# Kernel tuning notes

Measured on AMD Instinct MI355X. Metric: run time of the kernel, lower is better.

## Reference

```python
import jax, jax.numpy as jnp
import numpy as np

N_STEPS = 2   # n_steps; n_head = 1 (module is only consistent for a single head)
NEG_SLOPE = 0.2


def setup_inputs() -> dict:
    key = jax.random.key(0)
    ks = jax.random.split(key, 6)
    B, C, N = 8, 2048, 2048  # N must equal input_dim (coefs*out broadcast requirement)
    s = 1.0 / np.sqrt(C).astype(np.float32)
    x = jax.random.normal(ks[0], (B, C, N), jnp.float32)
    Wa = jax.random.normal(ks[1], (C, C), jnp.float32) * s   # conv1x1, no bias
    Wb = jax.random.normal(ks[2], (C,), jnp.float32) * s     # conv1x1 -> 1 channel
    bb = jnp.zeros((1,), jnp.float32)
    Wc = jax.random.normal(ks[3], (C,), jnp.float32) * s
    bc = jnp.zeros((1,), jnp.float32)
    bias = jnp.zeros((C,), jnp.float32)                      # self.bias (zeros)
    return dict(x=x, Wa=Wa, Wb=Wb, bb=bb, Wc=Wc, bc=bc, bias=bias)


def _head_attention(out, Wa, Wb, bb, Wc, bc, bias):
    # dropout p=0.0 -> identity
    h = jnp.einsum('oc,bcn->bon', Wa, out)            # [B,C,N] conv1x1 projection
    t1 = jnp.einsum('c,bcn->bn', Wb, h) + bb          # [B,N]
    t2 = jnp.einsum('c,bcn->bn', Wc, h) + bc          # [B,N]
    z = t1[:, None, :] + t2[:, :, None]               # [B,N,N] additive outer-sum
    z = jnp.where(z >= 0, z, NEG_SLOPE * z)           # leaky_relu(0.2)
    # torch F.softmax with no dim on a 3D tensor uses legacy dim=0 (batch dim)
    coefs = jax.nn.softmax(z, axis=0)
    re = coefs * h + bias                             # bias broadcasts over last axis
    return re                                         # [B,N,N] (== [B,C,N] since N==C)


def reference(x, Wa, Wb, bb, Wc, bc, bias):
    out = x
    for _ in range(N_STEPS):
        # n_head == 1: stack of one head then mean is the head itself
        out = _head_attention(out, Wa, Wb, bb, Wc, bc, bias)
    return out
```

## Files before the change

kernel.cpp:

```cpp
#include <hip/hip_runtime.h>
#include <hip/hip_bf16.h>

typedef unsigned short ushort_t;
typedef __attribute__((ext_vector_type(8))) short bf16x8;
typedef __attribute__((ext_vector_type(4))) float f32x4;
typedef __attribute__((ext_vector_type(8))) unsigned short u16x8;
typedef __attribute__((ext_vector_type(4))) unsigned short u16x4;

#define NDIM 2048
#define BDIM 8

__device__ __forceinline__ float bf2f(unsigned short u) {
  union { unsigned int i; float f; } v; v.i = ((unsigned int)u) << 16; return v.f;
}
__device__ __forceinline__ unsigned short f2bf(float f) {
  union { float f; unsigned int i; } v; v.f = f;
  unsigned int x = v.i;
  x += 0x7fffu + ((x >> 16) & 1u);
  return (unsigned short)(x >> 16);
}

__device__ __forceinline__ void gload16(const void* g, void* l) {
  __builtin_amdgcn_global_load_lds(
      (const __attribute__((address_space(1))) void*)g,
      (__attribute__((address_space(3))) void*)l,
      16, 0, 0);
}

__global__ __launch_bounds__(256) void convert_bf16(const float* __restrict__ src,
                                                    unsigned short* __restrict__ dst, int n) {
  int i = (blockIdx.x * 256 + threadIdx.x) * 4;
  if (i < n) {
    f32x4 v = *(const f32x4*)&src[i];
    u16x4 w;
    #pragma unroll
    for (int k = 0; k < 4; ++k) w[k] = f2bf(v[k]);
    *(u16x4*)&dst[i] = w;
  }
}

__global__ __launch_bounds__(256) void transpose_convert(const float* __restrict__ x,
                                                         unsigned short* __restrict__ dst) {
  __shared__ float tile[64][65];
  const int b  = blockIdx.z;
  const int n0 = blockIdx.x * 64;
  const int c0 = blockIdx.y * 64;
  const int tr = threadIdx.x >> 4;
  const int tc = threadIdx.x & 15;
  const float* src = x + ((size_t)b * NDIM + c0) * NDIM + n0;
  #pragma unroll
  for (int p = 0; p < 4; ++p) {
    int r = p * 16 + tr;
    f32x4 v = *(const f32x4*)&src[(size_t)r * NDIM + tc * 4];
    #pragma unroll
    for (int k = 0; k < 4; ++k) tile[r][tc * 4 + k] = v[k];
  }
  __syncthreads();
  unsigned short* d = dst + ((size_t)b * NDIM + n0) * NDIM + c0;
  #pragma unroll
  for (int p = 0; p < 4; ++p) {
    int r = p * 16 + tr;
    u16x4 w;
    #pragma unroll
    for (int k = 0; k < 4; ++k) w[k] = f2bf(tile[tc * 4 + k][r]);
    *(u16x4*)&d[(size_t)r * NDIM + tc * 4] = w;
  }
}

__global__ __launch_bounds__(256) void weff1(const float* __restrict__ Wa,
                                             const float* __restrict__ Wb,
                                             const float* __restrict__ Wc,
                                             float* __restrict__ part) {
  int c  = blockIdx.x * 256 + threadIdx.x;
  int o0 = blockIdx.y * 128;
  float ab = 0.f, ac = 0.f;
  for (int o = o0; o < o0 + 128; ++o) {
    float w = Wa[(size_t)o * NDIM + c];
    ab = fmaf(Wb[o], w, ab);
    ac = fmaf(Wc[o], w, ac);
  }
  part[(size_t)(blockIdx.y * 2 + 0) * NDIM + c] = ab;
  part[(size_t)(blockIdx.y * 2 + 1) * NDIM + c] = ac;
}
__global__ __launch_bounds__(256) void weff2(const float* __restrict__ part,
                                             float* __restrict__ wbe, float* __restrict__ wce) {
  int c = blockIdx.x * 256 + threadIdx.x;
  float ab = 0.f, ac = 0.f;
  #pragma unroll
  for (int i = 0; i < 16; ++i) {
    ab += part[(size_t)(i * 2 + 0) * NDIM + c];
    ac += part[(size_t)(i * 2 + 1) * NDIM + c];
  }
  wbe[c] = ab; wce[c] = ac;
}

__global__ __launch_bounds__(256) void t_kernel(const unsigned short* __restrict__ curT,
                                                const float* __restrict__ wbe,
                                                const float* __restrict__ wce,
                                                const float* __restrict__ bb,
                                                const float* __restrict__ bc,
                                                float* __restrict__ t1, float* __restrict__ t2) {
  int row  = blockIdx.x * 4 + (threadIdx.x >> 6);
  int lane = threadIdx.x & 63;
  const unsigned short* r = curT + (size_t)row * NDIM;
  float a1 = 0.f, a2 = 0.f;
  #pragma unroll
  for (int p = 0; p < 4; ++p) {
    int c0 = p * 512 + lane * 8;
    u16x8 v = *(const u16x8*)&r[c0];
    f32x4 w1a = *(const f32x4*)&wbe[c0];
    f32x4 w1b = *(const f32x4*)&wbe[c0 + 4];
    f32x4 w2a = *(const f32x4*)&wce[c0];
    f32x4 w2b = *(const f32x4*)&wce[c0 + 4];
    #pragma unroll
    for (int j = 0; j < 4; ++j) {
      float xv = bf2f(v[j]);
      a1 = fmaf(w1a[j], xv, a1);
      a2 = fmaf(w2a[j], xv, a2);
    }
    #pragma unroll
    for (int j = 0; j < 4; ++j) {
      float xv = bf2f(v[4 + j]);
      a1 = fmaf(w1b[j], xv, a1);
      a2 = fmaf(w2b[j], xv, a2);
    }
  }
  #pragma unroll
  for (int off = 32; off > 0; off >>= 1) {
    a1 += __shfl_xor(a1, off);
    a2 += __shfl_xor(a2, off);
  }
  if (lane == 0) { t1[row] = a1 + bb[0]; t2[row] = a2 + bc[0]; }
}

__global__ __launch_bounds__(256) void s_kernel(const float* __restrict__ t1,
                                                const float* __restrict__ t2,
                                                float* __restrict__ S) {
  int n = blockIdx.x * 256 + threadIdx.x;
  int o = blockIdx.y;
  float acc = 0.f;
  #pragma unroll
  for (int b = 0; b < BDIM; ++b) {
    float z = t1[b * NDIM + n] + t2[b * NDIM + o];
    z = z >= 0.f ? z : 0.2f * z;
    acc += __expf(z);
  }
  S[(size_t)o * NDIM + n] = __logf(acc);
}

__global__ __launch_bounds__(512, 2) void gemm_fused(
    const unsigned short* __restrict__ A,
    const unsigned short* __restrict__ Bt,
    const float* __restrict__ t1, const float* __restrict__ t2,
    const float* __restrict__ S,  const float* __restrict__ bias,
    unsigned short* __restrict__ outT,
    float* __restrict__ outF,
    int write_f32) {
  __shared__ __align__(16) unsigned short sbuf[4 * 16384];

  const int tid  = threadIdx.x;
  const int lane = tid & 63;
  const int w    = tid >> 6;
  const int wr   = w >> 2;
  const int wc   = w & 3;
  const int bn0  = blockIdx.x * 256;
  const int bm0  = blockIdx.y * 256;
  const int bz   = blockIdx.z;
  const unsigned short* Bb = Bt + (size_t)bz * NDIM * NDIM;

  f32x4 acc[8][4];
  #pragma unroll
  for (int m = 0; m < 8; ++m)
    #pragma unroll
    for (int n = 0; n < 4; ++n) acc[m][n] = (f32x4){0.f, 0.f, 0.f, 0.f};

  const int sr = lane >> 2;
  const int sc = lane & 3;
  const int r0 = (w * 2 + 0) * 16 + sr;
  const int r1 = (w * 2 + 1) * 16 + sr;
  const int sg = sc ^ ((r0 >> 1) & 3);
  const unsigned short* a0 = A  + (size_t)(bm0 + r0) * NDIM + sg * 8;
  const unsigned short* a1 = A  + (size_t)(bm0 + r1) * NDIM + sg * 8;
  const unsigned short* b0 = Bb + (size_t)(bn0 + r0) * NDIM + sg * 8;
  const unsigned short* b1 = Bb + (size_t)(bn0 + r1) * NDIM + sg * 8;

  auto stageA = [&](int kt, int buf) {
    gload16(a0 + kt, &sbuf[buf * 16384 + (w * 2 + 0) * 512]);
    gload16(a1 + kt, &sbuf[buf * 16384 + (w * 2 + 1) * 512]);
  };
  auto stageB = [&](int kt, int buf) {
    gload16(b0 + kt, &sbuf[buf * 16384 + 8192 + (w * 2 + 0) * 512]);
    gload16(b1 + kt, &sbuf[buf * 16384 + 8192 + (w * 2 + 1) * 512]);
  };

  const int fr = lane & 15;
  const int fs = lane >> 4;
  const int sp = (fs ^ ((fr >> 1) & 3)) * 8;

  stageA(0, 0);  stageB(0, 0);
  stageA(32, 1); stageB(32, 1);
  stageA(64, 2); stageB(64, 2);
  asm volatile("s_waitcnt vmcnt(8)" ::: "memory");
  __builtin_amdgcn_s_barrier();

  for (int t4 = 0; t4 < 64; t4 += 4) {
    #pragma unroll
    for (int u = 0; u < 4; ++u) {
      const int t  = t4 + u;
      const int cb = u;
      const int nb = (u + 3) & 3;
      const int tc = (t + 3 > 63) ? 63 : (t + 3);
      const int ktn = tc * 32;
      const unsigned short* Ab = &sbuf[cb * 16384];
      const unsigned short* Bl = &sbuf[cb * 16384 + 8192];

      bf16x8 av[4], bv[4];
      #pragma unroll
      for (int m = 0; m < 4; ++m)
        av[m] = *(const bf16x8*)&Ab[(wr * 128 + m * 16 + fr) * 32 + sp];
      #pragma unroll
      for (int n = 0; n < 4; ++n)
        bv[n] = *(const bf16x8*)&Bl[(wc * 64 + n * 16 + fr) * 32 + sp];
      stageA(ktn, nb);
      __builtin_amdgcn_s_barrier();
      __builtin_amdgcn_s_setprio(1);
      #pragma unroll
      for (int m = 0; m < 4; ++m)
        #pragma unroll
        for (int n = 0; n < 4; ++n)
          acc[m][n] = __builtin_amdgcn_mfma_f32_16x16x32_bf16(av[m], bv[n], acc[m][n], 0, 0, 0);
      __builtin_amdgcn_s_setprio(0);
      __builtin_amdgcn_s_barrier();

      #pragma unroll
      for (int m = 0; m < 4; ++m)
        av[m] = *(const bf16x8*)&Ab[(wr * 128 + (m + 4) * 16 + fr) * 32 + sp];
      stageB(ktn, nb);
      __builtin_amdgcn_s_barrier();
      __builtin_amdgcn_s_setprio(1);
      #pragma unroll
      for (int m = 0; m < 4; ++m)
        #pragma unroll
        for (int n = 0; n < 4; ++n)
          acc[m + 4][n] = __builtin_amdgcn_mfma_f32_16x16x32_bf16(av[m], bv[n], acc[m + 4][n], 0, 0, 0);
      __builtin_amdgcn_s_setprio(0);
      asm volatile("s_waitcnt vmcnt(8)" ::: "memory");
      __builtin_amdgcn_s_barrier();
    }
  }

  float* sT1f = (float*)&sbuf[3 * 16384];
  float* sT2f = sT1f + 256;
  if (tid < 256) sT1f[tid] = t1[bz * NDIM + bn0 + tid];
  else           sT2f[tid - 256] = t2[bz * NDIM + bm0 + (tid - 256)];
  __syncthreads();

  const int lr4 = fs * 4;
  #pragma unroll
  for (int m = 0; m < 8; ++m) {
    #pragma unroll
    for (int n = 0; n < 4; ++n) {
      const int oo = wr * 128 + m * 16 + lr4;
      const int nn = wc * 64 + n * 16 + fr;
      const int o  = bm0 + oo;
      const int ng = bn0 + nn;
      const float tz1  = sT1f[nn];
      const float bval = bias[ng];
      if (write_f32) {
        #pragma unroll
        for (int r = 0; r < 4; ++r) {
          float z = tz1 + sT2f[oo + r];
          z = z >= 0.f ? z : 0.2f * z;
          float coef = __expf(z - S[(size_t)(o + r) * NDIM + ng]);
          outF[(size_t)bz * NDIM * NDIM + (size_t)(o + r) * NDIM + ng] =
              fmaf(coef, acc[m][n][r], bval);
        }
      } else {
        u16x4 wv;
        #pragma unroll
        for (int r = 0; r < 4; ++r) {
          float z = tz1 + sT2f[oo + r];
          z = z >= 0.f ? z : 0.2f * z;
          float coef = __expf(z - S[(size_t)(o + r) * NDIM + ng]);
          wv[r] = f2bf(fmaf(coef, acc[m][n][r], bval));
        }
        *(u16x4*)&outT[(size_t)bz * NDIM * NDIM + (size_t)ng * NDIM + o] = wv;
      }
    }
  }
}

extern "C" void kernel_launch(void* const* d_in, const int* in_sizes, int n_in,
                              void* d_out, int out_size, void* d_ws, size_t ws_size,
                              hipStream_t stream) {
  const float* x    = (const float*)d_in[0];
  const float* Wa   = (const float*)d_in[1];
  const float* Wb   = (const float*)d_in[2];
  const float* bb   = (const float*)d_in[3];
  const float* Wc   = (const float*)d_in[4];
  const float* bc   = (const float*)d_in[5];
  const float* bias = (const float*)d_in[6];
  float* out = (float*)d_out;

  char* ws = (char*)d_ws;
  unsigned short* curA = (unsigned short*)ws; ws += (size_t)BDIM * NDIM * NDIM * 2;
  unsigned short* curB = (unsigned short*)ws; ws += (size_t)BDIM * NDIM * NDIM * 2;
  unsigned short* WaB  = (unsigned short*)ws; ws += (size_t)NDIM * NDIM * 2;
  float* t1   = (float*)ws; ws += (size_t)BDIM * NDIM * 4;
  float* t2   = (float*)ws; ws += (size_t)BDIM * NDIM * 4;
  float* wbe  = (float*)ws; ws += NDIM * 4;
  float* wce  = (float*)ws; ws += NDIM * 4;
  float* part = (float*)ws; ws += (size_t)32 * NDIM * 4;
  float* S    = (float*)ws; ws += (size_t)NDIM * NDIM * 4;

  convert_bf16<<<4096, 256, 0, stream>>>(Wa, WaB, NDIM * NDIM);
  transpose_convert<<<dim3(32, 32, BDIM), 256, 0, stream>>>(x, curA);
  weff1<<<dim3(8, 16), 256, 0, stream>>>(Wa, Wb, Wc, part);
  weff2<<<8, 256, 0, stream>>>(part, wbe, wce);

  for (int step = 0; step < 2; ++step) {
    const unsigned short* cur = step ? curB : curA;
    t_kernel<<<(BDIM * NDIM) / 4, 256, 0, stream>>>(cur, wbe, wce, bb, bc, t1, t2);
    s_kernel<<<dim3(NDIM / 256, NDIM), 256, 0, stream>>>(t1, t2, S);
    gemm_fused<<<dim3(8, 8, BDIM), 512, 0, stream>>>(
        WaB, cur, t1, t2, S, bias, curB, out, step);
  }
}
```

Baseline: 388.4 us.

## Remap GEMM blocks across XCDs and merge the two MFMA phases per k-step

The 3D grid becomes a 1D grid of 512 blocks. Block ids are remapped so that tiles sharing the same Wa row-block (bm) and batch region land on the same XCD, which should improve L2 reuse. The inner k-loop issues both A and B async stages up front, loads all LDS fragments at once, and runs all 32 MFMAs in a single phase. That removes two of the three barriers per k-step. The costs are more live fragment registers, and the per-u-iteration stage-then-single-barrier pattern needs the 4-buffer ring depth to stay race-free. The epilogue scratch moves to buffer 0.

```diff
diff --git a/kernel.cpp b/kernel.cpp
--- a/kernel.cpp
+++ b/kernel.cpp
@@ -158,14 +158,21 @@
     int write_f32) {
   __shared__ __align__(16) unsigned short sbuf[4 * 16384];
 
+  const int id   = blockIdx.x;
+  const int xcd  = id & 7;
+  const int j    = id >> 3;
+  const int bm   = (xcd >> 1) * 2 + (j & 1);
+  const int idx  = (xcd & 1) * 32 + (j >> 1);
+  const int bz   = idx >> 3;
+  const int bn   = idx & 7;
+  const int bn0  = bn * 256;
+  const int bm0  = bm * 256;
+
   const int tid  = threadIdx.x;
   const int lane = tid & 63;
   const int w    = tid >> 6;
   const int wr   = w >> 2;
   const int wc   = w & 3;
-  const int bn0  = blockIdx.x * 256;
-  const int bm0  = blockIdx.y * 256;
-  const int bz   = blockIdx.z;
   const unsigned short* Bb = Bt + (size_t)bz * NDIM * NDIM;
 
   f32x4 acc[8][4];
@@ -214,42 +221,39 @@
       const unsigned short* Ab = &sbuf[cb * 16384];
       const unsigned short* Bl = &sbuf[cb * 16384 + 8192];
 
-      bf16x8 av[4], bv[4];
+      stageA(ktn, nb);
+      stageB(ktn, nb);
+
+      bf16x8 av0[4], bv[4], av1[4];
       #pragma unroll
       for (int m = 0; m < 4; ++m)
-        av[m] = *(const bf16x8*)&Ab[(wr * 128 + m * 16 + fr) * 32 + sp];
+        av0[m] = *(const bf16x8*)&Ab[(wr * 128 + m * 16 + fr) * 32 + sp];
       #pragma unroll
       for (int n = 0; n < 4; ++n)
         bv[n] = *(const bf16x8*)&Bl[(wc * 64 + n * 16 + fr) * 32 + sp];
-      stageA(ktn, nb);
-      __builtin_amdgcn_s_barrier();
+      #pragma unroll
+      for (int m = 0; m < 4; ++m)
+        av1[m] = *(const bf16x8*)&Ab[(wr * 128 + (m + 4) * 16 + fr) * 32 + sp];
+
       __builtin_amdgcn_s_setprio(1);
       #pragma unroll
       for (int m = 0; m < 4; ++m)
         #pragma unroll
         for (int n = 0; n < 4; ++n)
-          acc[m][n] = __builtin_amdgcn_mfma_f32_16x16x32_bf16(av[m], bv[n], acc[m][n], 0, 0, 0);
-      __builtin_amdgcn_s_setprio(0);
-      __builtin_amdgcn_s_barrier();
-
-      #pragma unroll
-      for (int m = 0; m < 4; ++m)
-        av[m] = *(const bf16x8*)&Ab[(wr * 128 + (m + 4) * 16 + fr) * 32 + sp];
-      stageB(ktn, nb);
-      __builtin_amdgcn_s_barrier();
-      __builtin_amdgcn_s_setprio(1);
+          acc[m][n] = __builtin_amdgcn_mfma_f32_16x16x32_bf16(av0[m], bv[n], acc[m][n], 0, 0, 0);
       #pragma unroll
       for (int m = 0; m < 4; ++m)
         #pragma unroll
         for (int n = 0; n < 4; ++n)
-          acc[m + 4][n] = __builtin_amdgcn_mfma_f32_16x16x32_bf16(av[m], bv[n], acc[m + 4][n], 0, 0, 0);
+          acc[m + 4][n] = __builtin_amdgcn_mfma_f32_16x16x32_bf16(av1[m], bv[n], acc[m + 4][n], 0, 0, 0);
       __builtin_amdgcn_s_setprio(0);
+
       asm volatile("s_waitcnt vmcnt(8)" ::: "memory");
       __builtin_amdgcn_s_barrier();
     }
   }
 
-  float* sT1f = (float*)&sbuf[3 * 16384];
+  float* sT1f = (float*)&sbuf[0];
   float* sT2f = sT1f + 256;
   if (tid < 256) sT1f[tid] = t1[bz * NDIM + bn0 + tid];
   else           sT2f[tid - 256] = t2[bz * NDIM + bm0 + (tid - 256)];
@@ -322,7 +326,7 @@
     const unsigned short* cur = step ? curB : curA;
     t_kernel<<<(BDIM * NDIM) / 4, 256, 0, stream>>>(cur, wbe, wce, bb, bc, t1, t2);
     s_kernel<<<dim3(NDIM / 256, NDIM), 256, 0, stream>>>(t1, t2, S);
-    gemm_fused<<<dim3(8, 8, BDIM), 512, 0, stream>>>(
+    gemm_fused<<<512, 512, 0, stream>>>(
         WaB, cur, t1, t2, S, bias, curB, out, step);
   }
 }
```

Result: no change. 393.8 us (+1.4%).
